# Kernel tuning notes

Measured on AMD Instinct MI355X. Metric: run time of the kernel, lower is better.

Reference implementation:

```python
import jax, jax.numpy as jnp
import numpy as np

D = 4096
B = 4096


def build_H(n):
    # Sylvester Hadamard matrix, entries +-1, unnormalized (matches repo's build_H)
    H = jnp.ones((1, 1), jnp.float32)
    base = jnp.array([[1.0, 1.0], [1.0, -1.0]], jnp.float32)
    for _ in range(int(np.log2(n))):
        H = jnp.kron(base, H)
    return H


def fwht(x):
    # Unnormalized fast Walsh-Hadamard transform along the last axis.
    # fwht(v) == H @ v for Sylvester H. x: (..., n), n a power of two.
    shape = x.shape
    n = shape[-1]
    x = x.reshape(-1, n)
    h = 1
    while h < n:
        x = x.reshape(-1, n // (2 * h), 2, h)
        a = x[:, :, 0, :]
        b = x[:, :, 1, :]
        x = jnp.stack([a + b, a - b], axis=2).reshape(-1, n)
        h *= 2
    return x.reshape(shape)


def w_bar(u, s1, s2, H):
    # diag(s1) @ FWHT( diag(u) @ (H * s2) )  ==  diag(s1) H diag(u) H diag(s2)
    M = u[:, None] * (H * s2[None, :])          # (D, D)
    return s1[:, None] * fwht(M.T).T             # FWHT along axis 0 == H @ M


def setup_inputs() -> dict:
    key = jax.random.key(0)
    k0, k1, k2 = jax.random.split(key, 3)
    x = jax.random.normal(k0, (B, D), dtype=jnp.float32)
    epsilon = jax.random.normal(k1, (D,), dtype=jnp.float32)
    s1 = jnp.ones((D,), jnp.float32) * 0.01
    s2 = jnp.ones((D,), jnp.float32) * 0.01
    g_mu = jnp.zeros((D,), jnp.float32)
    g_rho = jax.random.uniform(k2, (D,), jnp.float32, minval=-5.0, maxval=-4.0)
    return {"x": x, "epsilon": epsilon, "s1": s1, "s2": s2, "g_mu": g_mu, "g_rho": g_rho}


def reference(x, epsilon, s1, s2, g_mu, g_rho):
    H = build_H(D)
    sigma = jax.nn.softplus(g_rho)               # g_sigma_sqrt_diagonal
    W = w_bar(g_mu, s1, s2, H) + w_bar(sigma * epsilon, s1, s2, H)  # (D, D)
    return x @ W.T                               # (B, D)
```

## Files before the change

### kernel.cpp

```cpp
#include <hip/hip_runtime.h>
#include <cstddef>

#define DSZ 4096

__global__ void compute_v_kernel(const float* __restrict__ eps,
                                 const float* __restrict__ g_mu,
                                 const float* __restrict__ g_rho,
                                 float* __restrict__ v) {
    int i = blockIdx.x * blockDim.x + threadIdx.x;
    if (i < DSZ) {
        float rho = g_rho[i];
        float sp = fmaxf(rho, 0.0f) + log1pf(expf(-fabsf(rho)));
        v[i] = g_mu[i] + sp * eps[i];
    }
}

__device__ __forceinline__ int swz(int a) {
    return a ^ (((a >> 6) & 15) << 2);
}

#define FWHT16(Y) do {                                                  \
    _Pragma("unroll")                                                   \
    for (int s_ = 1; s_ < 16; s_ <<= 1) {                               \
        _Pragma("unroll")                                               \
        for (int r_ = 0; r_ < 16; ++r_) {                               \
            if ((r_ & s_) == 0) {                                       \
                float a_ = Y[r_];                                       \
                float b_ = Y[r_ | s_];                                  \
                Y[r_]      = a_ + b_;                                   \
                Y[r_ | s_] = a_ - b_;                                   \
            }                                                           \
        }                                                               \
    }                                                                   \
} while (0)

__global__ __launch_bounds__(256, 8) void whvi_kernel(
        const float* __restrict__ x,
        const float* __restrict__ s1,
        const float* __restrict__ s2,
        const float* __restrict__ v,
        float* __restrict__ out) {
    __shared__ float lds[DSZ];
    const int T = threadIdx.x;
    const int b = blockIdx.x;
    float y[16];

    const float4* x4  = (const float4*)(x + (size_t)b * DSZ);
    const float4* s24 = (const float4*)s2;
    #pragma unroll
    for (int j = 0; j < 4; ++j) {
        float4 xv = x4[T + 256 * j];
        float4 sv = s24[T + 256 * j];
        y[4 * j + 0] = xv.x * sv.x;
        y[4 * j + 1] = xv.y * sv.y;
        y[4 * j + 2] = xv.z * sv.z;
        y[4 * j + 3] = xv.w * sv.w;
    }

    FWHT16(y);

    #pragma unroll
    for (int j = 0; j < 4; ++j) {
        *(float4*)&lds[swz(4 * T + 1024 * j)] =
            make_float4(y[4 * j], y[4 * j + 1], y[4 * j + 2], y[4 * j + 3]);
    }
    __syncthreads();
    #pragma unroll
    for (int r = 0; r < 16; ++r)
        y[r] = lds[swz((T & 3) + 4 * r + 64 * (T >> 2))];

    FWHT16(y);

    #pragma unroll
    for (int r = 0; r < 16; ++r)
        lds[swz((T & 3) + 4 * r + 64 * (T >> 2))] = y[r];
    __syncthreads();
    #pragma unroll
    for (int r = 0; r < 16; ++r)
        y[r] = lds[swz((T & 63) + 64 * r + 1024 * (T >> 6))];

    FWHT16(y);

    const float* vb = v + (T & 63) + 1024 * (T >> 6);
    #pragma unroll
    for (int r = 0; r < 16; ++r)
        y[r] *= vb[64 * r];

    FWHT16(y);

    #pragma unroll
    for (int r = 0; r < 16; ++r)
        lds[swz((T & 63) + 64 * r + 1024 * (T >> 6))] = y[r];
    __syncthreads();
    #pragma unroll
    for (int r = 0; r < 16; ++r)
        y[r] = lds[swz((T & 3) + 4 * r + 64 * (T >> 2))];

    FWHT16(y);

    #pragma unroll
    for (int r = 0; r < 16; ++r)
        lds[swz((T & 3) + 4 * r + 64 * (T >> 2))] = y[r];
    __syncthreads();
    #pragma unroll
    for (int j = 0; j < 4; ++j) {
        float4 t4 = *(const float4*)&lds[swz(4 * T + 1024 * j)];
        y[4 * j + 0] = t4.x;
        y[4 * j + 1] = t4.y;
        y[4 * j + 2] = t4.z;
        y[4 * j + 3] = t4.w;
    }

    FWHT16(y);

    const float4* s14 = (const float4*)s1;
    float4* o4 = (float4*)(out + (size_t)b * DSZ);
    #pragma unroll
    for (int j = 0; j < 4; ++j) {
        float4 sv = s14[T + 256 * j];
        float4 ov;
        ov.x = y[4 * j + 0] * sv.x;
        ov.y = y[4 * j + 1] * sv.y;
        ov.z = y[4 * j + 2] * sv.z;
        ov.w = y[4 * j + 3] * sv.w;
        o4[T + 256 * j] = ov;
    }
}

extern "C" void kernel_launch(void* const* d_in, const int* in_sizes, int n_in,
                              void* d_out, int out_size, void* d_ws, size_t ws_size,
                              hipStream_t stream) {
    const float* x     = (const float*)d_in[0];
    const float* eps   = (const float*)d_in[1];
    const float* s1    = (const float*)d_in[2];
    const float* s2    = (const float*)d_in[3];
    const float* g_mu  = (const float*)d_in[4];
    const float* g_rho = (const float*)d_in[5];
    float* out = (float*)d_out;
    float* v   = (float*)d_ws;

    compute_v_kernel<<<DSZ / 256, 256, 0, stream>>>(eps, g_mu, g_rho, v);
    whvi_kernel<<<4096, 256, 0, stream>>>(x, s1, s2, v, out);
}
```

Before: 129.1 us.

## Process two rows per block with prefetch of the next row and nontemporal stores

Each block now handles two consecutive rows. It loads the second row's x into registers during the first row's FWHT, reuses s2 from registers for both rows, and writes output with nontemporal stores. The grid is halved and the launch-bounds occupancy hint drops from 8 to 6 blocks per CU. The aim is to hide global load latency behind compute and to keep the output from polluting the cache, at the cost of more registers and fewer blocks in flight.

```diff
diff --git a/kernel.cpp b/kernel.cpp
--- a/kernel.cpp
+++ b/kernel.cpp
@@ -19,6 +19,14 @@
     return a ^ (((a >> 6) & 15) << 2);
 }
 
+typedef float fv4 __attribute__((ext_vector_type(4)));
+__device__ __forceinline__ void nt_store4(float* dst, float a, float b,
+                                          float c, float d) {
+    fv4 t;
+    t.x = a; t.y = b; t.z = c; t.w = d;
+    __builtin_nontemporal_store(t, (fv4*)dst);
+}
+
 #define FWHT16(Y) do {                                                  \
     _Pragma("unroll")                                                   \
     for (int s_ = 1; s_ < 16; s_ <<= 1) {                               \
@@ -34,35 +42,23 @@
     }                                                                   \
 } while (0)
 
-__global__ __launch_bounds__(256, 8) void whvi_kernel(
-        const float* __restrict__ x,
-        const float* __restrict__ s1,
-        const float* __restrict__ s2,
-        const float* __restrict__ v,
-        float* __restrict__ out) {
-    __shared__ float lds[DSZ];
-    const int T = threadIdx.x;
-    const int b = blockIdx.x;
-    float y[16];
-
-    const float4* x4  = (const float4*)(x + (size_t)b * DSZ);
-    const float4* s24 = (const float4*)s2;
-    #pragma unroll
-    for (int j = 0; j < 4; ++j) {
-        float4 xv = x4[T + 256 * j];
-        float4 sv = s24[T + 256 * j];
-        y[4 * j + 0] = xv.x * sv.x;
-        y[4 * j + 1] = xv.y * sv.y;
-        y[4 * j + 2] = xv.z * sv.z;
-        y[4 * j + 3] = xv.w * sv.w;
-    }
-
+template <bool PF>
+__device__ __forceinline__ void process_row(float* y, float* lds, int T,
+                                            const float* __restrict__ v,
+                                            const float* __restrict__ s1,
+                                            float* __restrict__ outrow,
+                                            const float4* __restrict__ x1,
+                                            float4* p) {
     FWHT16(y);
 
     #pragma unroll
-    for (int j = 0; j < 4; ++j) {
+    for (int j = 0; j < 4; ++j)
         *(float4*)&lds[swz(4 * T + 1024 * j)] =
             make_float4(y[4 * j], y[4 * j + 1], y[4 * j + 2], y[4 * j + 3]);
+    if (PF) {
+        #pragma unroll
+        for (int j = 0; j < 4; ++j)
+            p[j] = x1[T + 256 * j];
     }
     __syncthreads();
     #pragma unroll
@@ -114,17 +110,55 @@
     FWHT16(y);
 
     const float4* s14 = (const float4*)s1;
-    float4* o4 = (float4*)(out + (size_t)b * DSZ);
     #pragma unroll
     for (int j = 0; j < 4; ++j) {
         float4 sv = s14[T + 256 * j];
-        float4 ov;
-        ov.x = y[4 * j + 0] * sv.x;
-        ov.y = y[4 * j + 1] * sv.y;
-        ov.z = y[4 * j + 2] * sv.z;
-        ov.w = y[4 * j + 3] * sv.w;
-        o4[T + 256 * j] = ov;
+        nt_store4(outrow + 4 * (T + 256 * j),
+                  y[4 * j + 0] * sv.x, y[4 * j + 1] * sv.y,
+                  y[4 * j + 2] * sv.z, y[4 * j + 3] * sv.w);
     }
+}
+
+__global__ __launch_bounds__(256, 6) void whvi_kernel(
+        const float* __restrict__ x,
+        const float* __restrict__ s1,
+        const float* __restrict__ s2,
+        const float* __restrict__ v,
+        float* __restrict__ out) {
+    __shared__ float lds[DSZ];
+    const int T = threadIdx.x;
+    const size_t row0 = 2 * (size_t)blockIdx.x;
+
+    const float4* x0 = (const float4*)(x + row0 * DSZ);
+    const float4* x1 = (const float4*)(x + (row0 + 1) * DSZ);
+
+    const float4* s24 = (const float4*)s2;
+    float4 s2r[4];
+    #pragma unroll
+    for (int j = 0; j < 4; ++j)
+        s2r[j] = s24[T + 256 * j];
+
+    float y[16];
+    float4 p[4];
+
+    #pragma unroll
+    for (int j = 0; j < 4; ++j) {
+        float4 xv = x0[T + 256 * j];
+        y[4 * j + 0] = xv.x * s2r[j].x;
+        y[4 * j + 1] = xv.y * s2r[j].y;
+        y[4 * j + 2] = xv.z * s2r[j].z;
+        y[4 * j + 3] = xv.w * s2r[j].w;
+    }
+    process_row<true>(y, lds, T, v, s1, out + row0 * DSZ, x1, p);
+
+    #pragma unroll
+    for (int j = 0; j < 4; ++j) {
+        y[4 * j + 0] = p[j].x * s2r[j].x;
+        y[4 * j + 1] = p[j].y * s2r[j].y;
+        y[4 * j + 2] = p[j].z * s2r[j].z;
+        y[4 * j + 3] = p[j].w * s2r[j].w;
+    }
+    process_row<false>(y, lds, T, v, s1, out + (row0 + 1) * DSZ, x1, p);
 }
 
 extern "C" void kernel_launch(void* const* d_in, const int* in_sizes, int n_in,
@@ -140,5 +174,5 @@
     float* v   = (float*)d_ws;
 
     compute_v_kernel<<<DSZ / 256, 256, 0, stream>>>(eps, g_mu, g_rho, v);
-    whvi_kernel<<<4096, 256, 0, stream>>>(x, s1, s2, v, out);
+    whvi_kernel<<<DSZ / 2, 256, 0, stream>>>(x, s1, s2, v, out);
 }
```

New measurement: 176.4 us. 1.37x slower.
